# Kernel tuning notes

Hardware: AMD Instinct MI355X
Metric: run time of the kernel (lower is better)

The kernel has to match this reference:

```python
import jax, jax.numpy as jnp
import numpy as np

N_SAMPLE, N_RES = 1024, 4096

def setup_inputs() -> dict:
    key = jax.random.key(0)
    k1, k2 = jax.random.split(key)
    pred = jax.random.normal(k1, (N_SAMPLE, N_RES, 3), dtype=jnp.float32)
    true = jax.random.normal(k2, (N_RES, 3), dtype=jnp.float32)
    mask = jnp.ones((N_RES,), dtype=jnp.bool_)
    return {"pred_coordinate": pred, "true_coordinate": true, "coordinate_mask": mask}


def _tm_score(pred_coordinate, true_coordinate, coordinate_mask):
    # mask used as weights: identical to torch's boolean gather + reduce
    w = coordinate_mask.astype(jnp.float32)           # [L]
    Lt = jnp.sum(w)                                   # number of valid residues
    # d0 normalization (RNA uses protein formula), clamped at 0.5
    d0 = jnp.where(Lt <= 15.0, 0.5, 1.24 * jnp.cbrt(Lt - 15.0) - 1.8)
    d0 = jnp.maximum(d0, 0.5)
    d0_sq = d0 * d0

    wn = w / Lt                                       # normalized weights [L]
    true_mean = jnp.einsum('l,li->i', wn, true_coordinate)              # [3]
    pred_mean = jnp.einsum('l,sli->si', wn, pred_coordinate)            # [S,3]
    pred_c = pred_coordinate - pred_mean[:, None, :]                    # [S,L,3]
    true_c = true_coordinate - true_mean                                # [L,3]

    # Kabsch: covariance H_s = pred_c^T diag(w) true_c  -> [S,3,3]
    H = jnp.einsum('sli,l,lj->sij', pred_c, w, true_c)
    U, _, Vt = jnp.linalg.svd(H, full_matrices=False)
    V = jnp.swapaxes(Vt, -1, -2)
    # proper rotation (no reflection): flip sign of last singular vector if det<0
    det = jnp.linalg.det(jnp.einsum('sij,skj->sik', V, U))              # det(V U^T)
    D = jnp.stack([jnp.ones_like(det), jnp.ones_like(det), jnp.sign(det)], axis=-1)  # [S,3]
    R = jnp.einsum('sij,sj,skj->sik', V, D, U)        # R = V diag(D) U^T, [S,3,3]

    aligned = jnp.einsum('sij,slj->sli', R, pred_c) + true_mean         # [S,L,3]
    d_sq = jnp.sum((aligned - true_coordinate) ** 2, axis=-1)           # [S,L]
    terms = 1.0 / (1.0 + d_sq / d0_sq)
    tm = jnp.einsum('sl,l->s', terms, wn)             # masked mean -> [S]
    return tm


def reference(pred_coordinate, true_coordinate, coordinate_mask):
    return _tm_score(pred_coordinate, true_coordinate, coordinate_mask)
```

## Files before the change

kernel.cpp:

```cpp
#include <hip/hip_runtime.h>
#include <math.h>


#define NS        1024
#define NL        4096
#define TPB       256
#define CHUNK_RES 1024
#define NCHUNK    4

__device__ __forceinline__ float waveReduceSum(float v) {
    #pragma unroll
    for (int off = 32; off > 0; off >>= 1)
        v += __shfl_down(v, off, 64);
    return v;
}

__device__ __forceinline__ double det3(const double B[4][4],
                                       int r0, int r1, int r2,
                                       int c0, int c1, int c2) {
    return B[r0][c0]*(B[r1][c1]*B[r2][c2] - B[r1][c2]*B[r2][c1])
         - B[r0][c1]*(B[r1][c0]*B[r2][c2] - B[r1][c2]*B[r2][c0])
         + B[r0][c2]*(B[r1][c0]*B[r2][c1] - B[r1][c1]*B[r2][c0]);
}

__global__ __launch_bounds__(TPB, 4) void tm_fused(
    const float* __restrict__ pred, const float* __restrict__ tru,
    const int* __restrict__ mask, float* __restrict__ out)
{
    const int s    = blockIdx.x;
    const int tid  = threadIdx.x;
    const int wave = tid >> 6, lane = tid & 63;
    const float* ps = pred + (size_t)s * NL * 3;

    __shared__ float ldsP[CHUNK_RES * 3];
    __shared__ float ldsT[CHUNK_RES * 3];
    __shared__ float sred[4][18];

    float acc[18];
    #pragma unroll
    for (int i = 0; i < 18; ++i) acc[i] = 0.f;

    for (int k = 0; k < NCHUNK; ++k) {
        const float4* gp = (const float4*)(ps  + (size_t)k * CHUNK_RES * 3);
        const float4* gt = (const float4*)(tru + (size_t)k * CHUNK_RES * 3);
        float4* lp = (float4*)ldsP;
        float4* lt = (float4*)ldsT;
        #pragma unroll
        for (int j = 0; j < 3; ++j) {
            const int idx = wave * 192 + j * 64 + lane;
            lp[idx] = gp[idx];
            lt[idx] = gt[idx];
        }
        __syncthreads();

        const float4* rp = (const float4*)&ldsP[tid * 12];
        const float4* rt = (const float4*)&ldsT[tid * 12];
        const float4 q0 = rp[0], q1 = rp[1], q2 = rp[2];
        const float4 u0 = rt[0], u1 = rt[1], u2 = rt[2];
        const int4   mi = *(const int4*)(mask + k * CHUNK_RES + tid * 4);

        const float px[4] = {q0.x, q0.w, q1.z, q2.y};
        const float py[4] = {q0.y, q1.x, q1.w, q2.z};
        const float pz[4] = {q0.z, q1.y, q2.x, q2.w};
        const float tx[4] = {u0.x, u0.w, u1.z, u2.y};
        const float ty[4] = {u0.y, u1.x, u1.w, u2.z};
        const float tz[4] = {u0.z, u1.y, u2.x, u2.w};
        const float wm[4] = {mi.x ? 1.f : 0.f, mi.y ? 1.f : 0.f,
                             mi.z ? 1.f : 0.f, mi.w ? 1.f : 0.f};

        #pragma unroll
        for (int r = 0; r < 4; ++r) {
            const float w = wm[r];
            const float wpx = w * px[r], wpy = w * py[r], wpz = w * pz[r];
            acc[0] += w;
            acc[1] += w * tx[r]; acc[2] += w * ty[r]; acc[3] += w * tz[r];
            acc[4] += wpx; acc[5] += wpy; acc[6] += wpz;
            acc[7]  += wpx * tx[r]; acc[8]  += wpx * ty[r]; acc[9]  += wpx * tz[r];
            acc[10] += wpy * tx[r]; acc[11] += wpy * ty[r]; acc[12] += wpy * tz[r];
            acc[13] += wpz * tx[r]; acc[14] += wpz * ty[r]; acc[15] += wpz * tz[r];
            acc[16] += wpx * px[r] + wpy * py[r] + wpz * pz[r];
            acc[17] += w * (tx[r]*tx[r] + ty[r]*ty[r] + tz[r]*tz[r]);
        }
        __syncthreads();
    }

    #pragma unroll
    for (int i = 0; i < 18; ++i) {
        float r = waveReduceSum(acc[i]);
        if (lane == 0) sred[wave][i] = r;
    }
    __syncthreads();

    double S[18];
    #pragma unroll
    for (int i = 0; i < 18; ++i)
        S[i] = (double)sred[0][i] + (double)sred[1][i]
             + (double)sred[2][i] + (double)sred[3][i];

    const double Lt = S[0], invLt = 1.0 / Lt;
    const double tmxd = S[1]*invLt, tmyd = S[2]*invLt, tmzd = S[3]*invLt;
    const double pmxd = S[4]*invLt, pmyd = S[5]*invLt, pmzd = S[6]*invLt;

    double HA[3][3];
    const double Sp[3] = {S[4], S[5], S[6]};
    const double St[3] = {S[1], S[2], S[3]};
    #pragma unroll
    for (int i = 0; i < 3; ++i)
        #pragma unroll
        for (int j = 0; j < 3; ++j)
            HA[i][j] = (S[7 + i*3 + j] - Sp[i]*St[j]*invLt) * invLt;
    const double gA = (S[16] - (Sp[0]*Sp[0]+Sp[1]*Sp[1]+Sp[2]*Sp[2])*invLt) * invLt;
    const double gB = (S[17] - (St[0]*St[0]+St[1]*St[1]+St[2]*St[2])*invLt) * invLt;

    const double Sxx=HA[0][0], Sxy=HA[0][1], Sxz=HA[0][2];
    const double Syx=HA[1][0], Syy=HA[1][1], Syz=HA[1][2];
    const double Szx=HA[2][0], Szy=HA[2][1], Szz=HA[2][2];
    double K[4][4] = {
      { Sxx+Syy+Szz, Syz-Szy,      Szx-Sxz,      Sxy-Syx      },
      { Syz-Szy,     Sxx-Syy-Szz,  Sxy+Syx,      Szx+Sxz      },
      { Szx-Sxz,     Sxy+Syx,      Syy-Sxx-Szz,  Syz+Szy      },
      { Sxy-Syx,     Szx+Sxz,      Syz+Szy,      Szz-Sxx-Syy  }
    };

    double E2 = 0.0;
    #pragma unroll
    for (int i = 0; i < 4; ++i)
        #pragma unroll
        for (int j = 0; j < 4; ++j)
            if (j > i) E2 += K[i][i]*K[j][j] - K[i][j]*K[i][j];
    const double E3 = det3(K,1,2,3, 1,2,3) + det3(K,0,2,3, 0,2,3)
                    + det3(K,0,1,3, 0,1,3) + det3(K,0,1,2, 0,1,2);
    const double E4 = K[0][0]*det3(K,1,2,3, 1,2,3) - K[0][1]*det3(K,1,2,3, 0,2,3)
                    + K[0][2]*det3(K,1,2,3, 0,1,3) - K[0][3]*det3(K,1,2,3, 0,1,2);

    double lam = 0.5 * (gA + gB);
    #pragma unroll
    for (int it = 0; it < 8; ++it) {
        const double l2 = lam * lam;
        const double P  = ((l2 + E2) * lam - E3) * lam + E4;
        const double Pd = (4.0 * l2 + 2.0 * E2) * lam - E3;
        if (fabs(Pd) < 1e-300) break;
        lam -= P / Pd;
    }

    #pragma unroll
    for (int i = 0; i < 4; ++i) K[i][i] -= lam;
    double best[4] = {1.0, 0.0, 0.0, 0.0};
    double bestn = -1.0;
    #pragma unroll
    for (int r = 0; r < 4; ++r) {
        int ri[3]; int t = 0;
        #pragma unroll
        for (int i = 0; i < 4; ++i) if (i != r) ri[t++] = i;
        double v[4];
        #pragma unroll
        for (int c = 0; c < 4; ++c) {
            int cj[3]; t = 0;
            #pragma unroll
            for (int j = 0; j < 4; ++j) if (j != c) cj[t++] = j;
            const double d = det3(K, ri[0],ri[1],ri[2], cj[0],cj[1],cj[2]);
            v[c] = ((r + c) & 1) ? -d : d;
        }
        const double n = v[0]*v[0]+v[1]*v[1]+v[2]*v[2]+v[3]*v[3];
        if (n > bestn) { bestn = n; best[0]=v[0]; best[1]=v[1]; best[2]=v[2]; best[3]=v[3]; }
    }
    const double qn = 1.0 / sqrt(bestn);
    const double q0d = best[0]*qn, qxd = best[1]*qn, qyd = best[2]*qn, qzd = best[3]*qn;

    const float R00 = (float)(q0d*q0d+qxd*qxd-qyd*qyd-qzd*qzd);
    const float R01 = (float)(2.0*(qxd*qyd - q0d*qzd));
    const float R02 = (float)(2.0*(qxd*qzd + q0d*qyd));
    const float R10 = (float)(2.0*(qyd*qxd + q0d*qzd));
    const float R11 = (float)(q0d*q0d-qxd*qxd+qyd*qyd-qzd*qzd);
    const float R12 = (float)(2.0*(qyd*qzd - q0d*qxd));
    const float R20 = (float)(2.0*(qzd*qxd - q0d*qyd));
    const float R21 = (float)(2.0*(qzd*qyd + q0d*qxd));
    const float R22 = (float)(q0d*q0d-qxd*qxd-qyd*qyd+qzd*qzd);

    double d0 = (Lt <= 15.0) ? 0.5 : (1.24 * cbrt(Lt - 15.0) - 1.8);
    if (d0 < 0.5) d0 = 0.5;
    const float inv_d0sq = (float)(1.0 / (d0 * d0));
    const float invLtf   = (float)invLt;
    const float pmx = (float)pmxd, pmy = (float)pmyd, pmz = (float)pmzd;
    const float tmx = (float)tmxd, tmy = (float)tmyd, tmz = (float)tmzd;

    float tacc = 0.f;
    for (int k = 0; k < NCHUNK; ++k) {
        const float4* gp = (const float4*)(ps  + (size_t)k * CHUNK_RES * 3);
        const float4* gt = (const float4*)(tru + (size_t)k * CHUNK_RES * 3);
        float4* lp = (float4*)ldsP;
        float4* lt = (float4*)ldsT;
        #pragma unroll
        for (int j = 0; j < 3; ++j) {
            const int idx = wave * 192 + j * 64 + lane;
            lp[idx] = gp[idx];
            lt[idx] = gt[idx];
        }
        __syncthreads();

        const float4* rp = (const float4*)&ldsP[tid * 12];
        const float4* rt = (const float4*)&ldsT[tid * 12];
        const float4 q0 = rp[0], q1 = rp[1], q2 = rp[2];
        const float4 u0 = rt[0], u1 = rt[1], u2 = rt[2];
        const int4   mi = *(const int4*)(mask + k * CHUNK_RES + tid * 4);

        const float px[4] = {q0.x, q0.w, q1.z, q2.y};
        const float py[4] = {q0.y, q1.x, q1.w, q2.z};
        const float pz[4] = {q0.z, q1.y, q2.x, q2.w};
        const float tx[4] = {u0.x, u0.w, u1.z, u2.y};
        const float ty[4] = {u0.y, u1.x, u1.w, u2.z};
        const float tz[4] = {u0.z, u1.y, u2.x, u2.w};
        const float wm[4] = {mi.x ? 1.f : 0.f, mi.y ? 1.f : 0.f,
                             mi.z ? 1.f : 0.f, mi.w ? 1.f : 0.f};

        #pragma unroll
        for (int r = 0; r < 4; ++r) {
            const float vx = px[r] - pmx, vy = py[r] - pmy, vz = pz[r] - pmz;
            const float a0 = R00*vx + R01*vy + R02*vz + tmx - tx[r];
            const float a1 = R10*vx + R11*vy + R12*vz + tmy - ty[r];
            const float a2 = R20*vx + R21*vy + R22*vz + tmz - tz[r];
            const float dsq = a0*a0 + a1*a1 + a2*a2;
            tacc += wm[r] * __builtin_amdgcn_rcpf(1.0f + dsq * inv_d0sq);
        }
        __syncthreads();
    }
    tacc *= invLtf;

    float r = waveReduceSum(tacc);
    if (lane == 0) sred[wave][0] = r;
    __syncthreads();
    if (tid == 0)
        out[s] = sred[0][0] + sred[1][0] + sred[2][0] + sred[3][0];
}

extern "C" void kernel_launch(void* const* d_in, const int* in_sizes, int n_in,
                              void* d_out, int out_size, void* d_ws, size_t ws_size,
                              hipStream_t stream) {
    const float* pred = (const float*)d_in[0];
    const float* tru  = (const float*)d_in[1];
    const int*   mask = (const int*)d_in[2];
    float* out = (float*)d_out;
    (void)d_ws; (void)ws_size;
    tm_fused<<<NS, TPB, 0, stream>>>(pred, tru, mask, out);
}
```

Before: 99.14 us.

## Keep pred coordinates in registers, use float Jacobi eigen-solver, widen blocks

```diff
diff --git a/kernel.cpp b/kernel.cpp
--- a/kernel.cpp
+++ b/kernel.cpp
@@ -4,23 +4,16 @@
 
 #define NS        1024
 #define NL        4096
-#define TPB       256
-#define CHUNK_RES 1024
-#define NCHUNK    4
+#define TPB       512
+#define NCHUNK    2
+#define CHUNK_RES (NL / NCHUNK)
+#define NWAVE     (TPB / 64)
 
 __device__ __forceinline__ float waveReduceSum(float v) {
     #pragma unroll
     for (int off = 32; off > 0; off >>= 1)
         v += __shfl_down(v, off, 64);
     return v;
-}
-
-__device__ __forceinline__ double det3(const double B[4][4],
-                                       int r0, int r1, int r2,
-                                       int c0, int c1, int c2) {
-    return B[r0][c0]*(B[r1][c1]*B[r2][c2] - B[r1][c2]*B[r2][c1])
-         - B[r0][c1]*(B[r1][c0]*B[r2][c2] - B[r1][c2]*B[r2][c0])
-         + B[r0][c2]*(B[r1][c0]*B[r2][c1] - B[r1][c1]*B[r2][c0]);
 }
 
 __global__ __launch_bounds__(TPB, 4) void tm_fused(
@@ -34,20 +27,25 @@
 
     __shared__ float ldsP[CHUNK_RES * 3];
     __shared__ float ldsT[CHUNK_RES * 3];
-    __shared__ float sred[4][18];
-
-    float acc[18];
-    #pragma unroll
-    for (int i = 0; i < 18; ++i) acc[i] = 0.f;
-
+    __shared__ float sred[NWAVE][16];
+
+    float px[8], py[8], pz[8];
+    unsigned wmbits = 0;
+
+    float acc[16];
+    #pragma unroll
+    for (int i = 0; i < 16; ++i) acc[i] = 0.f;
+
+    #pragma unroll
     for (int k = 0; k < NCHUNK; ++k) {
-        const float4* gp = (const float4*)(ps  + (size_t)k * CHUNK_RES * 3);
-        const float4* gt = (const float4*)(tru + (size_t)k * CHUNK_RES * 3);
+        const int cbase = k * CHUNK_RES;
+        const float4* gp = (const float4*)(ps  + (size_t)cbase * 3);
+        const float4* gt = (const float4*)(tru + (size_t)cbase * 3);
         float4* lp = (float4*)ldsP;
         float4* lt = (float4*)ldsT;
         #pragma unroll
         for (int j = 0; j < 3; ++j) {
-            const int idx = wave * 192 + j * 64 + lane;
+            const int idx = j * TPB + tid;
             lp[idx] = gp[idx];
             lt[idx] = gt[idx];
         }
@@ -57,125 +55,117 @@
         const float4* rt = (const float4*)&ldsT[tid * 12];
         const float4 q0 = rp[0], q1 = rp[1], q2 = rp[2];
         const float4 u0 = rt[0], u1 = rt[1], u2 = rt[2];
-        const int4   mi = *(const int4*)(mask + k * CHUNK_RES + tid * 4);
-
-        const float px[4] = {q0.x, q0.w, q1.z, q2.y};
-        const float py[4] = {q0.y, q1.x, q1.w, q2.z};
-        const float pz[4] = {q0.z, q1.y, q2.x, q2.w};
-        const float tx[4] = {u0.x, u0.w, u1.z, u2.y};
-        const float ty[4] = {u0.y, u1.x, u1.w, u2.z};
-        const float tz[4] = {u0.z, u1.y, u2.x, u2.w};
-        const float wm[4] = {mi.x ? 1.f : 0.f, mi.y ? 1.f : 0.f,
-                             mi.z ? 1.f : 0.f, mi.w ? 1.f : 0.f};
+        const int4   mi = *(const int4*)(mask + cbase + tid * 4);
+
+        const float lpx[4] = {q0.x, q0.w, q1.z, q2.y};
+        const float lpy[4] = {q0.y, q1.x, q1.w, q2.z};
+        const float lpz[4] = {q0.z, q1.y, q2.x, q2.w};
+        const float ltx[4] = {u0.x, u0.w, u1.z, u2.y};
+        const float lty[4] = {u0.y, u1.x, u1.w, u2.z};
+        const float ltz[4] = {u0.z, u1.y, u2.x, u2.w};
+        const int   im[4]  = {mi.x, mi.y, mi.z, mi.w};
 
         #pragma unroll
         for (int r = 0; r < 4; ++r) {
-            const float w = wm[r];
-            const float wpx = w * px[r], wpy = w * py[r], wpz = w * pz[r];
+            const float w = im[r] ? 1.f : 0.f;
+            if (im[r]) wmbits |= (1u << (k * 4 + r));
+            px[k*4+r] = lpx[r]; py[k*4+r] = lpy[r]; pz[k*4+r] = lpz[r];
+            const float wpx = w * lpx[r], wpy = w * lpy[r], wpz = w * lpz[r];
             acc[0] += w;
-            acc[1] += w * tx[r]; acc[2] += w * ty[r]; acc[3] += w * tz[r];
+            acc[1] += w * ltx[r]; acc[2] += w * lty[r]; acc[3] += w * ltz[r];
             acc[4] += wpx; acc[5] += wpy; acc[6] += wpz;
-            acc[7]  += wpx * tx[r]; acc[8]  += wpx * ty[r]; acc[9]  += wpx * tz[r];
-            acc[10] += wpy * tx[r]; acc[11] += wpy * ty[r]; acc[12] += wpy * tz[r];
-            acc[13] += wpz * tx[r]; acc[14] += wpz * ty[r]; acc[15] += wpz * tz[r];
-            acc[16] += wpx * px[r] + wpy * py[r] + wpz * pz[r];
-            acc[17] += w * (tx[r]*tx[r] + ty[r]*ty[r] + tz[r]*tz[r]);
-        }
-        __syncthreads();
-    }
-
-    #pragma unroll
-    for (int i = 0; i < 18; ++i) {
+            acc[7]  += wpx * ltx[r]; acc[8]  += wpx * lty[r]; acc[9]  += wpx * ltz[r];
+            acc[10] += wpy * ltx[r]; acc[11] += wpy * lty[r]; acc[12] += wpy * ltz[r];
+            acc[13] += wpz * ltx[r]; acc[14] += wpz * lty[r]; acc[15] += wpz * ltz[r];
+        }
+        __syncthreads();
+    }
+
+    #pragma unroll
+    for (int i = 0; i < 16; ++i) {
         float r = waveReduceSum(acc[i]);
         if (lane == 0) sred[wave][i] = r;
     }
     __syncthreads();
 
-    double S[18];
-    #pragma unroll
-    for (int i = 0; i < 18; ++i)
-        S[i] = (double)sred[0][i] + (double)sred[1][i]
-             + (double)sred[2][i] + (double)sred[3][i];
+    double S[16];
+    #pragma unroll
+    for (int i = 0; i < 16; ++i) {
+        double t = 0.0;
+        #pragma unroll
+        for (int wv = 0; wv < NWAVE; ++wv) t += (double)sred[wv][i];
+        S[i] = t;
+    }
 
     const double Lt = S[0], invLt = 1.0 / Lt;
     const double tmxd = S[1]*invLt, tmyd = S[2]*invLt, tmzd = S[3]*invLt;
     const double pmxd = S[4]*invLt, pmyd = S[5]*invLt, pmzd = S[6]*invLt;
 
-    double HA[3][3];
-    const double Sp[3] = {S[4], S[5], S[6]};
-    const double St[3] = {S[1], S[2], S[3]};
-    #pragma unroll
-    for (int i = 0; i < 3; ++i)
-        #pragma unroll
-        for (int j = 0; j < 3; ++j)
-            HA[i][j] = (S[7 + i*3 + j] - Sp[i]*St[j]*invLt) * invLt;
-    const double gA = (S[16] - (Sp[0]*Sp[0]+Sp[1]*Sp[1]+Sp[2]*Sp[2])*invLt) * invLt;
-    const double gB = (S[17] - (St[0]*St[0]+St[1]*St[1]+St[2]*St[2])*invLt) * invLt;
-
-    const double Sxx=HA[0][0], Sxy=HA[0][1], Sxz=HA[0][2];
-    const double Syx=HA[1][0], Syy=HA[1][1], Syz=HA[1][2];
-    const double Szx=HA[2][0], Szy=HA[2][1], Szz=HA[2][2];
-    double K[4][4] = {
+    float H[3][3];
+    {
+        const double Sp[3] = {S[4], S[5], S[6]};
+        const double St[3] = {S[1], S[2], S[3]};
+        #pragma unroll
+        for (int i = 0; i < 3; ++i)
+            #pragma unroll
+            for (int j = 0; j < 3; ++j)
+                H[i][j] = (float)((S[7 + i*3 + j] - Sp[i]*St[j]*invLt) * invLt);
+    }
+
+    const float Sxx=H[0][0], Sxy=H[0][1], Sxz=H[0][2];
+    const float Syx=H[1][0], Syy=H[1][1], Syz=H[1][2];
+    const float Szx=H[2][0], Szy=H[2][1], Szz=H[2][2];
+    float A[4][4] = {
       { Sxx+Syy+Szz, Syz-Szy,      Szx-Sxz,      Sxy-Syx      },
       { Syz-Szy,     Sxx-Syy-Szz,  Sxy+Syx,      Szx+Sxz      },
       { Szx-Sxz,     Sxy+Syx,      Syy-Sxx-Szz,  Syz+Szy      },
       { Sxy-Syx,     Szx+Sxz,      Syz+Szy,      Szz-Sxx-Syy  }
     };
-
-    double E2 = 0.0;
-    #pragma unroll
-    for (int i = 0; i < 4; ++i)
-        #pragma unroll
-        for (int j = 0; j < 4; ++j)
-            if (j > i) E2 += K[i][i]*K[j][j] - K[i][j]*K[i][j];
-    const double E3 = det3(K,1,2,3, 1,2,3) + det3(K,0,2,3, 0,2,3)
-                    + det3(K,0,1,3, 0,1,3) + det3(K,0,1,2, 0,1,2);
-    const double E4 = K[0][0]*det3(K,1,2,3, 1,2,3) - K[0][1]*det3(K,1,2,3, 0,2,3)
-                    + K[0][2]*det3(K,1,2,3, 0,1,3) - K[0][3]*det3(K,1,2,3, 0,1,2);
-
-    double lam = 0.5 * (gA + gB);
-    #pragma unroll
-    for (int it = 0; it < 8; ++it) {
-        const double l2 = lam * lam;
-        const double P  = ((l2 + E2) * lam - E3) * lam + E4;
-        const double Pd = (4.0 * l2 + 2.0 * E2) * lam - E3;
-        if (fabs(Pd) < 1e-300) break;
-        lam -= P / Pd;
-    }
-
-    #pragma unroll
-    for (int i = 0; i < 4; ++i) K[i][i] -= lam;
-    double best[4] = {1.0, 0.0, 0.0, 0.0};
-    double bestn = -1.0;
-    #pragma unroll
-    for (int r = 0; r < 4; ++r) {
-        int ri[3]; int t = 0;
-        #pragma unroll
-        for (int i = 0; i < 4; ++i) if (i != r) ri[t++] = i;
-        double v[4];
-        #pragma unroll
-        for (int c = 0; c < 4; ++c) {
-            int cj[3]; t = 0;
-            #pragma unroll
-            for (int j = 0; j < 4; ++j) if (j != c) cj[t++] = j;
-            const double d = det3(K, ri[0],ri[1],ri[2], cj[0],cj[1],cj[2]);
-            v[c] = ((r + c) & 1) ? -d : d;
-        }
-        const double n = v[0]*v[0]+v[1]*v[1]+v[2]*v[2]+v[3]*v[3];
-        if (n > bestn) { bestn = n; best[0]=v[0]; best[1]=v[1]; best[2]=v[2]; best[3]=v[3]; }
-    }
-    const double qn = 1.0 / sqrt(bestn);
-    const double q0d = best[0]*qn, qxd = best[1]*qn, qyd = best[2]*qn, qzd = best[3]*qn;
-
-    const float R00 = (float)(q0d*q0d+qxd*qxd-qyd*qyd-qzd*qzd);
-    const float R01 = (float)(2.0*(qxd*qyd - q0d*qzd));
-    const float R02 = (float)(2.0*(qxd*qzd + q0d*qyd));
-    const float R10 = (float)(2.0*(qyd*qxd + q0d*qzd));
-    const float R11 = (float)(q0d*q0d-qxd*qxd+qyd*qyd-qzd*qzd);
-    const float R12 = (float)(2.0*(qyd*qzd - q0d*qxd));
-    const float R20 = (float)(2.0*(qzd*qxd - q0d*qyd));
-    const float R21 = (float)(2.0*(qzd*qyd + q0d*qxd));
-    const float R22 = (float)(q0d*q0d-qxd*qxd-qyd*qyd+qzd*qzd);
+    float V[4][4] = {{1,0,0,0},{0,1,0,0},{0,0,1,0},{0,0,0,1}};
+
+    for (int sweep = 0; sweep < 8; ++sweep) {
+        for (int p = 0; p < 3; ++p) for (int q = p+1; q < 4; ++q) {
+            const float apq = A[p][q];
+            if (fabsf(apq) < 1e-30f) continue;
+            const float tau = (A[q][q] - A[p][p]) / (2.0f * apq);
+            const float tt  = (tau >= 0.0f ? 1.0f : -1.0f)
+                              / (fabsf(tau) + sqrtf(1.0f + tau*tau));
+            const float cc  = 1.0f / sqrtf(1.0f + tt*tt);
+            const float sn  = tt * cc;
+            #pragma unroll
+            for (int m = 0; m < 4; ++m) {
+                const float akp = A[m][p], akq = A[m][q];
+                A[m][p] = cc*akp - sn*akq;
+                A[m][q] = sn*akp + cc*akq;
+            }
+            #pragma unroll
+            for (int m = 0; m < 4; ++m) {
+                const float apk = A[p][m], aqk = A[q][m];
+                A[p][m] = cc*apk - sn*aqk;
+                A[q][m] = sn*apk + cc*aqk;
+            }
+            #pragma unroll
+            for (int m = 0; m < 4; ++m) {
+                const float vkp = V[m][p], vkq = V[m][q];
+                V[m][p] = cc*vkp - sn*vkq;
+                V[m][q] = sn*vkp + cc*vkq;
+            }
+        }
+    }
+    int imax = 0;
+    #pragma unroll
+    for (int i = 1; i < 4; ++i) if (A[i][i] > A[imax][imax]) imax = i;
+    const float q0f = V[0][imax], qxf = V[1][imax], qyf = V[2][imax], qzf = V[3][imax];
+
+    const float R00 = q0f*q0f+qxf*qxf-qyf*qyf-qzf*qzf;
+    const float R01 = 2.0f*(qxf*qyf - q0f*qzf);
+    const float R02 = 2.0f*(qxf*qzf + q0f*qyf);
+    const float R10 = 2.0f*(qyf*qxf + q0f*qzf);
+    const float R11 = q0f*q0f-qxf*qxf+qyf*qyf-qzf*qzf;
+    const float R12 = 2.0f*(qyf*qzf - q0f*qxf);
+    const float R20 = 2.0f*(qzf*qxf - q0f*qyf);
+    const float R21 = 2.0f*(qzf*qyf + q0f*qxf);
+    const float R22 = q0f*q0f-qxf*qxf-qyf*qyf+qzf*qzf;
 
     double d0 = (Lt <= 15.0) ? 0.5 : (1.24 * cbrt(Lt - 15.0) - 1.8);
     if (d0 < 0.5) d0 = 0.5;
@@ -185,42 +175,33 @@
     const float tmx = (float)tmxd, tmy = (float)tmyd, tmz = (float)tmzd;
 
     float tacc = 0.f;
+    #pragma unroll
     for (int k = 0; k < NCHUNK; ++k) {
-        const float4* gp = (const float4*)(ps  + (size_t)k * CHUNK_RES * 3);
-        const float4* gt = (const float4*)(tru + (size_t)k * CHUNK_RES * 3);
-        float4* lp = (float4*)ldsP;
+        const int cbase = k * CHUNK_RES;
+        const float4* gt = (const float4*)(tru + (size_t)cbase * 3);
         float4* lt = (float4*)ldsT;
         #pragma unroll
         for (int j = 0; j < 3; ++j) {
-            const int idx = wave * 192 + j * 64 + lane;
-            lp[idx] = gp[idx];
+            const int idx = j * TPB + tid;
             lt[idx] = gt[idx];
         }
         __syncthreads();
 
-        const float4* rp = (const float4*)&ldsP[tid * 12];
         const float4* rt = (const float4*)&ldsT[tid * 12];
-        const float4 q0 = rp[0], q1 = rp[1], q2 = rp[2];
         const float4 u0 = rt[0], u1 = rt[1], u2 = rt[2];
-        const int4   mi = *(const int4*)(mask + k * CHUNK_RES + tid * 4);
-
-        const float px[4] = {q0.x, q0.w, q1.z, q2.y};
-        const float py[4] = {q0.y, q1.x, q1.w, q2.z};
-        const float pz[4] = {q0.z, q1.y, q2.x, q2.w};
-        const float tx[4] = {u0.x, u0.w, u1.z, u2.y};
-        const float ty[4] = {u0.y, u1.x, u1.w, u2.z};
-        const float tz[4] = {u0.z, u1.y, u2.x, u2.w};
-        const float wm[4] = {mi.x ? 1.f : 0.f, mi.y ? 1.f : 0.f,
-                             mi.z ? 1.f : 0.f, mi.w ? 1.f : 0.f};
+        const float ltx[4] = {u0.x, u0.w, u1.z, u2.y};
+        const float lty[4] = {u0.y, u1.x, u1.w, u2.z};
+        const float ltz[4] = {u0.z, u1.y, u2.x, u2.w};
 
         #pragma unroll
         for (int r = 0; r < 4; ++r) {
-            const float vx = px[r] - pmx, vy = py[r] - pmy, vz = pz[r] - pmz;
-            const float a0 = R00*vx + R01*vy + R02*vz + tmx - tx[r];
-            const float a1 = R10*vx + R11*vy + R12*vz + tmy - ty[r];
-            const float a2 = R20*vx + R21*vy + R22*vz + tmz - tz[r];
+            const float w = (wmbits >> (k * 4 + r)) & 1u ? 1.f : 0.f;
+            const float vx = px[k*4+r] - pmx, vy = py[k*4+r] - pmy, vz = pz[k*4+r] - pmz;
+            const float a0 = R00*vx + R01*vy + R02*vz + tmx - ltx[r];
+            const float a1 = R10*vx + R11*vy + R12*vz + tmy - lty[r];
+            const float a2 = R20*vx + R21*vy + R22*vz + tmz - ltz[r];
             const float dsq = a0*a0 + a1*a1 + a2*a2;
-            tacc += wm[r] * __builtin_amdgcn_rcpf(1.0f + dsq * inv_d0sq);
+            tacc += w * __builtin_amdgcn_rcpf(1.0f + dsq * inv_d0sq);
         }
         __syncthreads();
     }
@@ -229,8 +210,12 @@
     float r = waveReduceSum(tacc);
     if (lane == 0) sred[wave][0] = r;
     __syncthreads();
-    if (tid == 0)
-        out[s] = sred[0][0] + sred[1][0] + sred[2][0] + sred[3][0];
+    if (tid == 0) {
+        float t = 0.f;
+        #pragma unroll
+        for (int wv = 0; wv < NWAVE; ++wv) t += sred[wv][0];
+        out[s] = t;
+    }
 }
 
 extern "C" void kernel_launch(void* const* d_in, const int* in_sizes, int n_in,
```

New measurement: 270.5 us. +172.9%, slower.
